# Performance work log

Hardware: AMD Instinct MI355X
Metric: run time of the kernel (lower is better)

The kernel has to match this reference:

```python
import jax, jax.numpy as jnp
import numpy as np

B, S, D, H = 4, 2048, 1024, 16
HD = D // H  # head dim = 64


def setup_inputs() -> dict:
    key = jax.random.key(0)
    ks = jax.random.split(key, 11)
    sc = 1.0 / np.sqrt(D)
    return {
        "q": jax.random.normal(ks[0], (B, S, D), jnp.float32),
        "k": jax.random.normal(ks[1], (B, S, D), jnp.float32),
        "v": jax.random.normal(ks[2], (B, S, D), jnp.float32),
        "w_q": jax.random.normal(ks[3], (D, D), jnp.float32) * sc,
        "b_q": jnp.zeros((D,), jnp.float32),
        "w_k": jax.random.normal(ks[4], (D, D), jnp.float32) * sc,
        "b_k": jnp.zeros((D,), jnp.float32),
        "w_v": jax.random.normal(ks[5], (D, D), jnp.float32) * sc,
        "b_v": jnp.zeros((D,), jnp.float32),
        "w_fc": jax.random.normal(ks[6], (D, D), jnp.float32) * sc,
        "b_fc": jnp.zeros((D,), jnp.float32),
    }


def reference(q, k, v, w_q, b_q, w_k, b_k, w_v, b_v, w_fc, b_fc):
    scale = jnp.asarray(np.sqrt(HD), q.dtype)
    # QKV projections: [B,S,D] @ [D,D]^T (torch Linear: x @ W^T + b)
    Q = (q @ w_q.T + b_q).reshape(B, S, H, HD).transpose(0, 2, 1, 3)  # [B,H,S,HD]
    K = (k @ w_k.T + b_k).reshape(B, S, H, HD).transpose(0, 2, 1, 3)
    V = (v @ w_v.T + b_v).reshape(B, S, H, HD).transpose(0, 2, 1, 3)
    energy = jnp.einsum('bhqd,bhkd->bhqk', Q, K) / scale  # [B,H,S,S]
    attn = jax.nn.softmax(energy, axis=-1)  # dropout is identity in eval / p=0
    x = jnp.einsum('bhqk,bhkd->bhqd', attn, V)  # [B,H,S,HD]
    x = x.transpose(0, 2, 1, 3).reshape(B, S, D)
    return x @ w_fc.T + b_fc
```

## Files before the change

### kernel.cpp

```cpp
#include <hip/hip_runtime.h>
#include <stdint.h>

#define BN 4
#define SEQ 2048
#define DM 1024
#define NH 16
#define HD 64
#define ROWS (BN*SEQ)

typedef float  f32x4  __attribute__((ext_vector_type(4)));
typedef __bf16 bf16x8 __attribute__((ext_vector_type(8)));
typedef __bf16 bf16x4 __attribute__((ext_vector_type(4)));

__device__ inline bf16x8 cvt8(const float* __restrict__ src) {
    float4 x0 = *(const float4*)src;
    float4 x1 = *(const float4*)(src + 4);
    bf16x8 r;
    r[0] = (__bf16)x0.x; r[1] = (__bf16)x0.y; r[2] = (__bf16)x0.z; r[3] = (__bf16)x0.w;
    r[4] = (__bf16)x1.x; r[5] = (__bf16)x1.y; r[6] = (__bf16)x1.z; r[7] = (__bf16)x1.w;
    return r;
}

__device__ inline void gl_lds16(const void* g, void* l) {
    __builtin_amdgcn_global_load_lds((const __attribute__((address_space(1))) uint32_t*)g,
                                     (__attribute__((address_space(3))) uint32_t*)l, 16, 0, 0);
}

__global__ __launch_bounds__(256) void cast3(
    const float* __restrict__ a0, const float* __restrict__ a1, const float* __restrict__ a2,
    __bf16* __restrict__ o0, __bf16* __restrict__ o1, __bf16* __restrict__ o2, int n8) {
    int t = blockIdx.x * 256 + threadIdx.x;
    if (t >= n8) return;
    const float* in = (blockIdx.y == 0) ? a0 : (blockIdx.y == 1) ? a1 : a2;
    __bf16* out     = (blockIdx.y == 0) ? o0 : (blockIdx.y == 1) ? o1 : o2;
    *(bf16x8*)&out[(size_t)t * 8] = cvt8(&in[(size_t)t * 8]);
}

__global__ __launch_bounds__(256) void cast4(
    const float* __restrict__ a0, const float* __restrict__ a1,
    const float* __restrict__ a2, const float* __restrict__ a3,
    __bf16* __restrict__ o0, __bf16* __restrict__ o1,
    __bf16* __restrict__ o2, __bf16* __restrict__ o3, int n8) {
    int t = blockIdx.x * 256 + threadIdx.x;
    if (t >= n8) return;
    const float* in = (blockIdx.y == 0) ? a0 : (blockIdx.y == 1) ? a1 : (blockIdx.y == 2) ? a2 : a3;
    __bf16* out     = (blockIdx.y == 0) ? o0 : (blockIdx.y == 1) ? o1 : (blockIdx.y == 2) ? o2 : o3;
    *(bf16x8*)&out[(size_t)t * 8] = cvt8(&in[(size_t)t * 8]);
}

#define GEMM_CORE_GLDS(Xp, Wp)                                                     \
    __shared__ __align__(16) __bf16 As[128 * 32];                                  \
    __shared__ __align__(16) __bf16 Bs[128 * 32];                                  \
    const int tid  = threadIdx.x;                                                  \
    const int lane = tid & 63;                                                     \
    const int wave = tid >> 6;                                                     \
    const int wm = (wave >> 1) * 64;                                               \
    const int wn = (wave & 1) * 64;                                                \
    const int c16 = lane & 15;                                                     \
    const int g8  = (lane >> 4) * 8;                                               \
    const int row0 = blockIdx.x * 128;                                             \
    const int col0 = blockIdx.y * 128;                                             \
    f32x4 acc[4][4] = {};                                                          \
    for (int k0 = 0; k0 < DM; k0 += 32) {                                          \
        __syncthreads();                                                           \
        _Pragma("unroll")                                                          \
        for (int h = 0; h < 2; h++) {                                              \
            int cidx = h * 256 + tid;                                              \
            gl_lds16(&Xp[(size_t)(row0 + (cidx >> 2)) * DM + k0 + (cidx & 3) * 8], \
                     &As[(size_t)(h * 256 + wave * 64) * 8]);                      \
            gl_lds16(&Wp[(size_t)(col0 + (cidx >> 2)) * DM + k0 + (cidx & 3) * 8], \
                     &Bs[(size_t)(h * 256 + wave * 64) * 8]);                      \
        }                                                                          \
        __syncthreads();                                                           \
        bf16x8 a[4], bfr[4];                                                       \
        _Pragma("unroll")                                                          \
        for (int i = 0; i < 4; i++) a[i]   = *(const bf16x8*)&As[(wm + i * 16 + c16) * 32 + g8]; \
        _Pragma("unroll")                                                          \
        for (int i = 0; i < 4; i++) bfr[i] = *(const bf16x8*)&Bs[(wn + i * 16 + c16) * 32 + g8]; \
        _Pragma("unroll")                                                          \
        for (int mi = 0; mi < 4; mi++)                                             \
            _Pragma("unroll")                                                      \
            for (int ni = 0; ni < 4; ni++)                                         \
                acc[mi][ni] = __builtin_amdgcn_mfma_f32_16x16x32_bf16(a[mi], bfr[ni], acc[mi][ni], 0, 0, 0); \
    }

__global__ __launch_bounds__(256) void gemm_qk_f(
    const __bf16* __restrict__ qb, const __bf16* __restrict__ kb,
    const __bf16* __restrict__ wqb, const __bf16* __restrict__ wkb,
    const float* __restrict__ bq, const float* __restrict__ bk,
    __bf16* __restrict__ Qp, __bf16* __restrict__ Kp)
{
    const int z = blockIdx.z;
    const __bf16* X = z ? kb : qb;
    const __bf16* W = z ? wkb : wqb;
    const float* bias = z ? bk : bq;
    __bf16* O = z ? Kp : Qp;

    GEMM_CORE_GLDS(X, W)

    #pragma unroll
    for (int mi = 0; mi < 4; mi++) {
        int r0 = row0 + wm + mi * 16 + (lane >> 4) * 4;
        #pragma unroll
        for (int ni = 0; ni < 4; ni++) {
            int col = col0 + wn + ni * 16 + c16;
            float bsv = bias[col];
            int h = col >> 6, d = col & 63;
            #pragma unroll
            for (int i = 0; i < 4; i++) {
                int r = r0 + i; int b = r >> 11, s = r & 2047;
                O[((size_t)(b * NH + h) * SEQ + s) * HD + d] = (__bf16)(acc[mi][ni][i] + bsv);
            }
        }
    }
}

__global__ __launch_bounds__(256) void gemm_v_f(
    const __bf16* __restrict__ vb, const __bf16* __restrict__ wvb,
    const float* __restrict__ bv, __bf16* __restrict__ Vt)
{
    GEMM_CORE_GLDS(vb, wvb)

    #pragma unroll
    for (int mi = 0; mi < 4; mi++) {
        int r0 = row0 + wm + mi * 16 + (lane >> 4) * 4;
        #pragma unroll
        for (int ni = 0; ni < 4; ni++) {
            int col = col0 + wn + ni * 16 + c16;
            float bsv = bv[col];
            int h = col >> 6, d = col & 63;
            int b = r0 >> 11, s0 = r0 & 2047;
            size_t base = ((size_t)((b * NH + h) * HD + d)) * SEQ + s0;
            #pragma unroll
            for (int i = 0; i < 4; i++)
                Vt[base + i] = (__bf16)(acc[mi][ni][i] + bsv);
        }
    }
}

__global__ __launch_bounds__(256) void gemm_fc_f(
    const __bf16* __restrict__ Xc, const __bf16* __restrict__ Wfb,
    const float* __restrict__ bias, float* __restrict__ out)
{
    GEMM_CORE_GLDS(Xc, Wfb)

    #pragma unroll
    for (int mi = 0; mi < 4; mi++) {
        int r0 = row0 + wm + mi * 16 + (lane >> 4) * 4;
        #pragma unroll
        for (int ni = 0; ni < 4; ni++) {
            int col = col0 + wn + ni * 16 + c16;
            float bsv = bias[col];
            #pragma unroll
            for (int i = 0; i < 4; i++)
                out[(size_t)(r0 + i) * DM + col] = acc[mi][ni][i] + bsv;
        }
    }
}

__global__ __launch_bounds__(256) void gemm_qk(
    const __bf16* __restrict__ qb, const __bf16* __restrict__ kb,
    const float* __restrict__ wqf, const float* __restrict__ wkf,
    const float* __restrict__ bq, const float* __restrict__ bk,
    __bf16* __restrict__ Qp, __bf16* __restrict__ Kp)
{
    const int z = blockIdx.z;
    const __bf16* X = z ? kb : qb;
    const float* W  = z ? wkf : wqf;
    const float* bias = z ? bk : bq;
    __bf16* O = z ? Kp : Qp;

    __shared__ __align__(16) __bf16 As[128 * 32];
    __shared__ __align__(16) __bf16 Bs[128 * 32];

    const int tid  = threadIdx.x;
    const int lane = tid & 63;
    const int wave = tid >> 6;
    const int wm = (wave >> 1) * 64;
    const int wn = (wave & 1) * 64;
    const int c16 = lane & 15;
    const int g8  = (lane >> 4) * 8;
    const int row0 = blockIdx.x * 128;
    const int col0 = blockIdx.y * 128;
    const int brow = tid >> 1;
    const int bcc  = (tid & 1) * 16;

    f32x4 acc[4][4] = {};
    for (int k0 = 0; k0 < DM; k0 += 32) {
        __syncthreads();
        #pragma unroll
        for (int h = 0; h < 2; h++) {
            int cidx = h * 256 + tid;
            gl_lds16(&X[(size_t)(row0 + (cidx >> 2)) * DM + k0 + (cidx & 3) * 8],
                     &As[(size_t)(h * 256 + wave * 64) * 8]);
        }
        *(bf16x8*)&Bs[brow * 32 + bcc]     = cvt8(&W[(size_t)(col0 + brow) * DM + k0 + bcc]);
        *(bf16x8*)&Bs[brow * 32 + bcc + 8] = cvt8(&W[(size_t)(col0 + brow) * DM + k0 + bcc + 8]);
        __syncthreads();

        bf16x8 a[4], bfr[4];
        #pragma unroll
        for (int i = 0; i < 4; i++) a[i]   = *(const bf16x8*)&As[(wm + i * 16 + c16) * 32 + g8];
        #pragma unroll
        for (int i = 0; i < 4; i++) bfr[i] = *(const bf16x8*)&Bs[(wn + i * 16 + c16) * 32 + g8];
        #pragma unroll
        for (int mi = 0; mi < 4; mi++)
            #pragma unroll
            for (int ni = 0; ni < 4; ni++)
                acc[mi][ni] = __builtin_amdgcn_mfma_f32_16x16x32_bf16(a[mi], bfr[ni], acc[mi][ni], 0, 0, 0);
    }

    #pragma unroll
    for (int mi = 0; mi < 4; mi++) {
        int r0 = row0 + wm + mi * 16 + (lane >> 4) * 4;
        #pragma unroll
        for (int ni = 0; ni < 4; ni++) {
            int col = col0 + wn + ni * 16 + c16;
            float bsv = bias[col];
            int h = col >> 6, d = col & 63;
            #pragma unroll
            for (int i = 0; i < 4; i++) {
                int r = r0 + i; int b = r >> 11, s = r & 2047;
                O[((size_t)(b * NH + h) * SEQ + s) * HD + d] = (__bf16)(acc[mi][ni][i] + bsv);
            }
        }
    }
}

__global__ __launch_bounds__(256) void gemm_v(
    const float* __restrict__ vf, const float* __restrict__ wvf,
    const float* __restrict__ bv, __bf16* __restrict__ Vt)
{
    __shared__ __align__(16) __bf16 As[128 * 32];
    __shared__ __align__(16) __bf16 Bs[128 * 32];

    const int tid  = threadIdx.x;
    const int lane = tid & 63;
    const int wave = tid >> 6;
    const int wm = (wave >> 1) * 64;
    const int wn = (wave & 1) * 64;
    const int c16 = lane & 15;
    const int g8  = (lane >> 4) * 8;
    const int row0 = blockIdx.x * 128;
    const int col0 = blockIdx.y * 128;
    const int brow = tid >> 1;
    const int bcc  = (tid & 1) * 16;

    f32x4 acc[4][4] = {};
    for (int k0 = 0; k0 < DM; k0 += 32) {
        __syncthreads();
        *(bf16x8*)&As[brow * 32 + bcc]     = cvt8(&vf[(size_t)(row0 + brow) * DM + k0 + bcc]);
        *(bf16x8*)&As[brow * 32 + bcc + 8] = cvt8(&vf[(size_t)(row0 + brow) * DM + k0 + bcc + 8]);
        *(bf16x8*)&Bs[brow * 32 + bcc]     = cvt8(&wvf[(size_t)(col0 + brow) * DM + k0 + bcc]);
        *(bf16x8*)&Bs[brow * 32 + bcc + 8] = cvt8(&wvf[(size_t)(col0 + brow) * DM + k0 + bcc + 8]);
        __syncthreads();

        bf16x8 a[4], bfr[4];
        #pragma unroll
        for (int i = 0; i < 4; i++) a[i]   = *(const bf16x8*)&As[(wm + i * 16 + c16) * 32 + g8];
        #pragma unroll
        for (int i = 0; i < 4; i++) bfr[i] = *(const bf16x8*)&Bs[(wn + i * 16 + c16) * 32 + g8];
        #pragma unroll
        for (int mi = 0; mi < 4; mi++)
            #pragma unroll
            for (int ni = 0; ni < 4; ni++)
                acc[mi][ni] = __builtin_amdgcn_mfma_f32_16x16x32_bf16(a[mi], bfr[ni], acc[mi][ni], 0, 0, 0);
    }

    #pragma unroll
    for (int mi = 0; mi < 4; mi++) {
        int r0 = row0 + wm + mi * 16 + (lane >> 4) * 4;
        #pragma unroll
        for (int ni = 0; ni < 4; ni++) {
            int col = col0 + wn + ni * 16 + c16;
            float bsv = bv[col];
            int h = col >> 6, d = col & 63;
            int b = r0 >> 11, s0 = r0 & 2047;
            size_t base = ((size_t)((b * NH + h) * HD + d)) * SEQ + s0;
            #pragma unroll
            for (int i = 0; i < 4; i++)
                Vt[base + i] = (__bf16)(acc[mi][ni][i] + bsv);
        }
    }
}

__global__ __launch_bounds__(256) void gemm_fc(
    const __bf16* __restrict__ Xc, const float* __restrict__ Wf,
    const float* __restrict__ bias, float* __restrict__ out)
{
    __shared__ __align__(16) __bf16 As[128 * 32];
    __shared__ __align__(16) __bf16 Bs[128 * 32];

    const int tid  = threadIdx.x;
    const int lane = tid & 63;
    const int wave = tid >> 6;
    const int wm = (wave >> 1) * 64;
    const int wn = (wave & 1) * 64;
    const int c16 = lane & 15;
    const int g8  = (lane >> 4) * 8;
    const int row0 = blockIdx.x * 128;
    const int col0 = blockIdx.y * 128;
    const int brow = tid >> 1;
    const int bcc  = (tid & 1) * 16;

    f32x4 acc[4][4] = {};
    for (int k0 = 0; k0 < DM; k0 += 32) {
        __syncthreads();
        #pragma unroll
        for (int h = 0; h < 2; h++) {
            int cidx = h * 256 + tid;
            gl_lds16(&Xc[(size_t)(row0 + (cidx >> 2)) * DM + k0 + (cidx & 3) * 8],
                     &As[(size_t)(h * 256 + wave * 64) * 8]);
        }
        *(bf16x8*)&Bs[brow * 32 + bcc]     = cvt8(&Wf[(size_t)(col0 + brow) * DM + k0 + bcc]);
        *(bf16x8*)&Bs[brow * 32 + bcc + 8] = cvt8(&Wf[(size_t)(col0 + brow) * DM + k0 + bcc + 8]);
        __syncthreads();

        bf16x8 a[4], bfr[4];
        #pragma unroll
        for (int i = 0; i < 4; i++) a[i]   = *(const bf16x8*)&As[(wm + i * 16 + c16) * 32 + g8];
        #pragma unroll
        for (int i = 0; i < 4; i++) bfr[i] = *(const bf16x8*)&Bs[(wn + i * 16 + c16) * 32 + g8];
        #pragma unroll
        for (int mi = 0; mi < 4; mi++)
            #pragma unroll
            for (int ni = 0; ni < 4; ni++)
                acc[mi][ni] = __builtin_amdgcn_mfma_f32_16x16x32_bf16(a[mi], bfr[ni], acc[mi][ni], 0, 0, 0);
    }

    #pragma unroll
    for (int mi = 0; mi < 4; mi++) {
        int r0 = row0 + wm + mi * 16 + (lane >> 4) * 4;
        #pragma unroll
        for (int ni = 0; ni < 4; ni++) {
            int col = col0 + wn + ni * 16 + c16;
            float bsv = bias[col];
            #pragma unroll
            for (int i = 0; i < 4; i++)
                out[(size_t)(r0 + i) * DM + col] = acc[mi][ni][i] + bsv;
        }
    }
}

__global__ __launch_bounds__(256, 4) void attn_kernel(
    const __bf16* __restrict__ Qp, const __bf16* __restrict__ Kp,
    const __bf16* __restrict__ Vt, __bf16* __restrict__ ctx)
{
    __shared__ __align__(16) __bf16 Ks[64 * 64];
    __shared__ __align__(16) __bf16 Vs[64 * 64];
    __shared__ __align__(16) __bf16 Ps[4][32 * 64];

    const int tid  = threadIdx.x;
    const int lane = tid & 63;
    const int w    = tid >> 6;
    const int bh   = blockIdx.y;
    const int q0   = blockIdx.x * 128 + w * 32;

    const __bf16* Qb = Qp + (size_t)bh * SEQ * HD;
    const __bf16* Kb = Kp + (size_t)bh * SEQ * HD;
    const __bf16* Vb = Vt + (size_t)bh * HD * SEQ;

    const int c16 = lane & 15;
    const int g   = lane >> 4;
    const int sw  = c16 & 7;

    bf16x8 qf[2][2];
    #pragma unroll
    for (int qs = 0; qs < 2; qs++)
        #pragma unroll
        for (int kc = 0; kc < 2; kc++)
            qf[qs][kc] = *(const bf16x8*)&Qb[(size_t)(q0 + qs * 16 + c16) * HD + kc * 32 + g * 8];

    float lp[2] = {0.f, 0.f};
    f32x4 o[4][2] = {};
    const float SC = 0.18033688f;

    const int srow = (w * 16) + (lane >> 3);
    const int sj   = (lane & 7) ^ (lane >> 3);

    for (int kt = 0; kt < SEQ / 64; kt++) {
        const int k0 = kt * 64;
        __syncthreads();
        #pragma unroll
        for (int h = 0; h < 2; h++) {
            int r = srow + h * 8;
            gl_lds16(&Kb[(size_t)(k0 + r) * HD + sj * 8], &Ks[(size_t)(w * 16 + h * 8) * 64]);
            gl_lds16(&Vb[(size_t)r * SEQ + k0 + sj * 8],  &Vs[(size_t)(w * 16 + h * 8) * 64]);
        }
        __syncthreads();

        f32x4 sc[4][2] = {};
        #pragma unroll
        for (int t = 0; t < 4; t++) {
            #pragma unroll
            for (int kc = 0; kc < 2; kc++) {
                bf16x8 kf = *(const bf16x8*)&Ks[(t * 16 + c16) * 64 + ((kc * 4 + g) ^ sw) * 8];
                sc[t][0] = __builtin_amdgcn_mfma_f32_16x16x32_bf16(kf, qf[0][kc], sc[t][0], 0, 0, 0);
                sc[t][1] = __builtin_amdgcn_mfma_f32_16x16x32_bf16(kf, qf[1][kc], sc[t][1], 0, 0, 0);
            }
        }

        #pragma unroll
        for (int qs = 0; qs < 2; qs++) {
            float ps = 0.f;
            #pragma unroll
            for (int t = 0; t < 4; t++) {
                bf16x4 pk;
                #pragma unroll
                for (int i = 0; i < 4; i++) {
                    float pv = exp2f(sc[t][qs][i] * SC);
                    ps += pv;
                    pk[i] = (__bf16)pv;
                }
                *(bf16x4*)&Ps[w][(qs * 16 + c16) * 64 + ((2 * t + (g >> 1)) ^ sw) * 8 + (g & 1) * 4] = pk;
            }
            lp[qs] += ps;
        }

        bf16x8 pf[2][2];
        #pragma unroll
        for (int qs = 0; qs < 2; qs++)
            #pragma unroll
            for (int kc = 0; kc < 2; kc++)
                pf[qs][kc] = *(const bf16x8*)&Ps[w][(qs * 16 + c16) * 64 + ((kc * 4 + g) ^ sw) * 8];

        #pragma unroll
        for (int t = 0; t < 4; t++) {
            #pragma unroll
            for (int kc = 0; kc < 2; kc++) {
                bf16x8 vfr = *(const bf16x8*)&Vs[(t * 16 + c16) * 64 + ((kc * 4 + g) ^ sw) * 8];
                o[t][0] = __builtin_amdgcn_mfma_f32_16x16x32_bf16(vfr, pf[0][kc], o[t][0], 0, 0, 0);
                o[t][1] = __builtin_amdgcn_mfma_f32_16x16x32_bf16(vfr, pf[1][kc], o[t][1], 0, 0, 0);
            }
        }
    }

    const int hh = bh & (NH - 1);
    const int bb = bh >> 4;
    #pragma unroll
    for (int qs = 0; qs < 2; qs++) {
        float l = lp[qs];
        l += __shfl_xor(l, 16, 64);
        l += __shfl_xor(l, 32, 64);
        float inv = 1.f / l;
        int s = q0 + qs * 16 + c16;
        #pragma unroll
        for (int t = 0; t < 4; t++) {
            bf16x4 ov;
            #pragma unroll
            for (int i = 0; i < 4; i++) ov[i] = (__bf16)(o[t][qs][i] * inv);
            *(bf16x4*)&ctx[((size_t)(bb * SEQ + s)) * DM + hh * HD + t * 16 + g * 4] = ov;
        }
    }
}

extern "C" void kernel_launch(void* const* d_in, const int* in_sizes, int n_in,
                              void* d_out, int out_size, void* d_ws, size_t ws_size,
                              hipStream_t stream) {
    const float* q    = (const float*)d_in[0];
    const float* k    = (const float*)d_in[1];
    const float* v    = (const float*)d_in[2];
    const float* w_q  = (const float*)d_in[3];
    const float* b_q  = (const float*)d_in[4];
    const float* w_k  = (const float*)d_in[5];
    const float* b_k  = (const float*)d_in[6];
    const float* w_v  = (const float*)d_in[7];
    const float* b_v  = (const float*)d_in[8];
    const float* w_fc = (const float*)d_in[9];
    const float* b_fc = (const float*)d_in[10];
    float* out = (float*)d_out;

    __bf16* qb = (__bf16*)d_out;
    __bf16* kb = qb + (size_t)ROWS * DM;

    char* p = (char*)d_ws;
    auto alloc = [&](size_t bytes) { char* r = p; p += (bytes + 255) & ~(size_t)255; return r; };
    const size_t XSZ = (size_t)ROWS * DM * 2;
    const size_t WSZ = (size_t)DM * DM * 2;

    __bf16* Qp  = (__bf16*)alloc(XSZ);
    __bf16* Kp  = (__bf16*)alloc(XSZ);
    __bf16* Vt  = (__bf16*)alloc(XSZ);
    __bf16* ctx = (__bf16*)alloc(XSZ);

    const size_t base_need = (size_t)(p - (char*)d_ws);
    const size_t fast_need = base_need + 4 * (WSZ + 256);

    const int n8x = ROWS * DM / 8;
    const int n8w = DM * DM / 8;

    __bf16* vb = Qp;

    cast3<<<dim3(n8x / 256, 3), 256, 0, stream>>>(q, k, v, qb, kb, vb, n8x);

    if (ws_size >= fast_need) {
        __bf16* wqb  = (__bf16*)alloc(WSZ);
        __bf16* wkb  = (__bf16*)alloc(WSZ);
        __bf16* wvb  = (__bf16*)alloc(WSZ);
        __bf16* wfcb = (__bf16*)alloc(WSZ);

        cast4<<<dim3(n8w / 256, 4), 256, 0, stream>>>(
            w_q, w_k, w_v, w_fc, wqb, wkb, wvb, wfcb, n8w);

        gemm_v_f<<<dim3(ROWS / 128, DM / 128), 256, 0, stream>>>(vb, wvb, b_v, Vt);
        gemm_qk_f<<<dim3(ROWS / 128, DM / 128, 2), 256, 0, stream>>>(
            qb, kb, wqb, wkb, b_q, b_k, Qp, Kp);

        attn_kernel<<<dim3(SEQ / 128, BN * NH), 256, 0, stream>>>(Qp, Kp, Vt, ctx);

        gemm_fc_f<<<dim3(ROWS / 128, DM / 128), 256, 0, stream>>>(ctx, wfcb, b_fc, out);
    } else {
        gemm_v<<<dim3(ROWS / 128, DM / 128), 256, 0, stream>>>(v, w_v, b_v, Vt);
        gemm_qk<<<dim3(ROWS / 128, DM / 128, 2), 256, 0, stream>>>(
            qb, kb, w_q, w_k, b_q, b_k, Qp, Kp);

        attn_kernel<<<dim3(SEQ / 128, BN * NH), 256, 0, stream>>>(Qp, Kp, Vt, ctx);

        gemm_fc<<<dim3(ROWS / 128, DM / 128), 256, 0, stream>>>(ctx, w_fc, b_fc, out);
    }
}
```

Measured before the change: 365.6 us.

## Rewrite attention with 32x32 MFMA, register-resident P, and double-buffered K/V

```diff
diff --git a/kernel.cpp b/kernel.cpp
--- a/kernel.cpp
+++ b/kernel.cpp
@@ -9,8 +9,13 @@
 #define ROWS (BN*SEQ)
 
 typedef float  f32x4  __attribute__((ext_vector_type(4)));
+typedef float  f32x16 __attribute__((ext_vector_type(16)));
 typedef __bf16 bf16x8 __attribute__((ext_vector_type(8)));
 typedef __bf16 bf16x4 __attribute__((ext_vector_type(4)));
+typedef __bf16 bf16x2 __attribute__((ext_vector_type(2)));
+typedef unsigned int u32x4 __attribute__((ext_vector_type(4)));
+
+#define QSCALE 0.18033688f
 
 __device__ inline bf16x8 cvt8(const float* __restrict__ src) {
     float4 x0 = *(const float4*)src;
@@ -95,6 +100,7 @@
     const __bf16* W = z ? wkb : wqb;
     const float* bias = z ? bk : bq;
     __bf16* O = z ? Kp : Qp;
+    const float qsc = z ? 1.0f : QSCALE;
 
     GEMM_CORE_GLDS(X, W)
 
@@ -109,7 +115,7 @@
             #pragma unroll
             for (int i = 0; i < 4; i++) {
                 int r = r0 + i; int b = r >> 11, s = r & 2047;
-                O[((size_t)(b * NH + h) * SEQ + s) * HD + d] = (__bf16)(acc[mi][ni][i] + bsv);
+                O[((size_t)(b * NH + h) * SEQ + s) * HD + d] = (__bf16)((acc[mi][ni][i] + bsv) * qsc);
             }
         }
     }
@@ -169,6 +175,7 @@
     const float* W  = z ? wkf : wqf;
     const float* bias = z ? bk : bq;
     __bf16* O = z ? Kp : Qp;
+    const float qsc = z ? 1.0f : QSCALE;
 
     __shared__ __align__(16) __bf16 As[128 * 32];
     __shared__ __align__(16) __bf16 Bs[128 * 32];
@@ -221,7 +228,7 @@
             #pragma unroll
             for (int i = 0; i < 4; i++) {
                 int r = r0 + i; int b = r >> 11, s = r & 2047;
-                O[((size_t)(b * NH + h) * SEQ + s) * HD + d] = (__bf16)(acc[mi][ni][i] + bsv);
+                O[((size_t)(b * NH + h) * SEQ + s) * HD + d] = (__bf16)((acc[mi][ni][i] + bsv) * qsc);
             }
         }
     }
@@ -342,13 +349,37 @@
     }
 }
 
-__global__ __launch_bounds__(256, 4) void attn_kernel(
+#define SOFTMAX_PACK(SV, PA0, PA1) do {                                            \
+    float p[16]; float ps = 0.f;                                                   \
+    _Pragma("unroll")                                                              \
+    for (int r = 0; r < 16; r++) { float pv = exp2f(SV[r]); p[r] = pv; ps += pv; } \
+    lp += ps;                                                                      \
+    unsigned pw[8];                                                                \
+    _Pragma("unroll")                                                              \
+    for (int i = 0; i < 8; i++) {                                                  \
+        bf16x2 t; t[0] = (__bf16)p[2*i]; t[1] = (__bf16)p[2*i+1];                  \
+        pw[i] = __builtin_bit_cast(unsigned, t);                                   \
+    }                                                                              \
+    unsigned e0 = (unsigned)__shfl_xor((int)pw[0], 32, 64);                        \
+    unsigned e1 = (unsigned)__shfl_xor((int)pw[1], 32, 64);                        \
+    unsigned e2 = (unsigned)__shfl_xor((int)pw[2], 32, 64);                        \
+    unsigned e3 = (unsigned)__shfl_xor((int)pw[3], 32, 64);                        \
+    unsigned e4 = (unsigned)__shfl_xor((int)pw[4], 32, 64);                        \
+    unsigned e5 = (unsigned)__shfl_xor((int)pw[5], 32, 64);                        \
+    unsigned e6 = (unsigned)__shfl_xor((int)pw[6], 32, 64);                        \
+    unsigned e7 = (unsigned)__shfl_xor((int)pw[7], 32, 64);                        \
+    u32x4 wlo = { hi ? e2 : pw[0], hi ? e3 : pw[1], hi ? pw[2] : e0, hi ? pw[3] : e1 }; \
+    u32x4 whi = { hi ? e6 : pw[4], hi ? e7 : pw[5], hi ? pw[6] : e4, hi ? pw[7] : e5 }; \
+    PA0 = __builtin_bit_cast(bf16x8, wlo);                                         \
+    PA1 = __builtin_bit_cast(bf16x8, whi);                                         \
+} while (0)
+
+__global__ __launch_bounds__(256) void attn_kernel(
     const __bf16* __restrict__ Qp, const __bf16* __restrict__ Kp,
     const __bf16* __restrict__ Vt, __bf16* __restrict__ ctx)
 {
-    __shared__ __align__(16) __bf16 Ks[64 * 64];
-    __shared__ __align__(16) __bf16 Vs[64 * 64];
-    __shared__ __align__(16) __bf16 Ps[4][32 * 64];
+    __shared__ __align__(16) __bf16 Ks[2][64 * 64];
+    __shared__ __align__(16) __bf16 Vs[2][64 * 64];
 
     const int tid  = threadIdx.x;
     const int lane = tid & 63;
@@ -360,97 +391,86 @@
     const __bf16* Kb = Kp + (size_t)bh * SEQ * HD;
     const __bf16* Vb = Vt + (size_t)bh * HD * SEQ;
 
-    const int c16 = lane & 15;
-    const int g   = lane >> 4;
-    const int sw  = c16 & 7;
-
-    bf16x8 qf[2][2];
-    #pragma unroll
-    for (int qs = 0; qs < 2; qs++)
-        #pragma unroll
-        for (int kc = 0; kc < 2; kc++)
-            qf[qs][kc] = *(const bf16x8*)&Qb[(size_t)(q0 + qs * 16 + c16) * HD + kc * 32 + g * 8];
-
-    float lp[2] = {0.f, 0.f};
-    f32x4 o[4][2] = {};
-    const float SC = 0.18033688f;
-
-    const int srow = (w * 16) + (lane >> 3);
+    const int c32 = lane & 31;
+    const int hi  = lane >> 5;
+    const int sw  = c32 & 7;
+
+    bf16x8 qf[4];
+    #pragma unroll
+    for (int kc = 0; kc < 4; kc++)
+        qf[kc] = *(const bf16x8*)&Qb[(size_t)(q0 + c32) * HD + kc * 16 + hi * 8];
+
+    f32x16 o0 = {}, o1 = {};
+    float lp = 0.f;
+
+    const int srow = w * 16 + (lane >> 3);
     const int sj   = (lane & 7) ^ (lane >> 3);
 
-    for (int kt = 0; kt < SEQ / 64; kt++) {
+    auto stage = [&](int kt, int buf) {
         const int k0 = kt * 64;
-        __syncthreads();
         #pragma unroll
         for (int h = 0; h < 2; h++) {
             int r = srow + h * 8;
-            gl_lds16(&Kb[(size_t)(k0 + r) * HD + sj * 8], &Ks[(size_t)(w * 16 + h * 8) * 64]);
-            gl_lds16(&Vb[(size_t)r * SEQ + k0 + sj * 8],  &Vs[(size_t)(w * 16 + h * 8) * 64]);
-        }
-        __syncthreads();
-
-        f32x4 sc[4][2] = {};
-        #pragma unroll
-        for (int t = 0; t < 4; t++) {
-            #pragma unroll
-            for (int kc = 0; kc < 2; kc++) {
-                bf16x8 kf = *(const bf16x8*)&Ks[(t * 16 + c16) * 64 + ((kc * 4 + g) ^ sw) * 8];
-                sc[t][0] = __builtin_amdgcn_mfma_f32_16x16x32_bf16(kf, qf[0][kc], sc[t][0], 0, 0, 0);
-                sc[t][1] = __builtin_amdgcn_mfma_f32_16x16x32_bf16(kf, qf[1][kc], sc[t][1], 0, 0, 0);
-            }
-        }
-
-        #pragma unroll
-        for (int qs = 0; qs < 2; qs++) {
-            float ps = 0.f;
-            #pragma unroll
-            for (int t = 0; t < 4; t++) {
-                bf16x4 pk;
-                #pragma unroll
-                for (int i = 0; i < 4; i++) {
-                    float pv = exp2f(sc[t][qs][i] * SC);
-                    ps += pv;
-                    pk[i] = (__bf16)pv;
-                }
-                *(bf16x4*)&Ps[w][(qs * 16 + c16) * 64 + ((2 * t + (g >> 1)) ^ sw) * 8 + (g & 1) * 4] = pk;
-            }
-            lp[qs] += ps;
-        }
-
-        bf16x8 pf[2][2];
-        #pragma unroll
-        for (int qs = 0; qs < 2; qs++)
-            #pragma unroll
-            for (int kc = 0; kc < 2; kc++)
-                pf[qs][kc] = *(const bf16x8*)&Ps[w][(qs * 16 + c16) * 64 + ((kc * 4 + g) ^ sw) * 8];
-
-        #pragma unroll
-        for (int t = 0; t < 4; t++) {
-            #pragma unroll
-            for (int kc = 0; kc < 2; kc++) {
-                bf16x8 vfr = *(const bf16x8*)&Vs[(t * 16 + c16) * 64 + ((kc * 4 + g) ^ sw) * 8];
-                o[t][0] = __builtin_amdgcn_mfma_f32_16x16x32_bf16(vfr, pf[0][kc], o[t][0], 0, 0, 0);
-                o[t][1] = __builtin_amdgcn_mfma_f32_16x16x32_bf16(vfr, pf[1][kc], o[t][1], 0, 0, 0);
-            }
-        }
-    }
-
+            gl_lds16(&Kb[(size_t)(k0 + r) * HD + sj * 8], &Ks[buf][(w * 16 + h * 8) * 64]);
+            gl_lds16(&Vb[(size_t)r * SEQ + k0 + sj * 8],  &Vs[buf][(w * 16 + h * 8) * 64]);
+        }
+    };
+
+    const int NT = SEQ / 64;
+    stage(0, 0);
+    int cur = 0;
+
+    for (int kt = 0; kt < NT; kt++) {
+        __syncthreads();
+        if (kt + 1 < NT) stage(kt + 1, cur ^ 1);
+
+        const __bf16* ksb = &Ks[cur][0];
+        const __bf16* vsb = &Vs[cur][0];
+
+        f32x16 s0v = {}, s1v = {};
+        __builtin_amdgcn_s_setprio(1);
+        #pragma unroll
+        for (int kc = 0; kc < 4; kc++) {
+            bf16x8 kf0 = *(const bf16x8*)&ksb[(c32)      * 64 + (((kc << 1) | hi) ^ sw) * 8];
+            bf16x8 kf1 = *(const bf16x8*)&ksb[(32 + c32) * 64 + (((kc << 1) | hi) ^ sw) * 8];
+            s0v = __builtin_amdgcn_mfma_f32_32x32x16_bf16(kf0, qf[kc], s0v, 0, 0, 0);
+            s1v = __builtin_amdgcn_mfma_f32_32x32x16_bf16(kf1, qf[kc], s1v, 0, 0, 0);
+        }
+        __builtin_amdgcn_s_setprio(0);
+
+        bf16x8 pa[4];
+        SOFTMAX_PACK(s0v, pa[0], pa[1]);
+        SOFTMAX_PACK(s1v, pa[2], pa[3]);
+
+        __builtin_amdgcn_s_setprio(1);
+        #pragma unroll
+        for (int ks = 0; ks < 4; ks++) {
+            bf16x8 vf0 = *(const bf16x8*)&vsb[(c32)      * 64 + (((ks << 1) | hi) ^ sw) * 8];
+            bf16x8 vf1 = *(const bf16x8*)&vsb[(32 + c32) * 64 + (((ks << 1) | hi) ^ sw) * 8];
+            o0 = __builtin_amdgcn_mfma_f32_32x32x16_bf16(vf0, pa[ks], o0, 0, 0, 0);
+            o1 = __builtin_amdgcn_mfma_f32_32x32x16_bf16(vf1, pa[ks], o1, 0, 0, 0);
+        }
+        __builtin_amdgcn_s_setprio(0);
+
+        cur ^= 1;
+    }
+
+    float l = lp + __shfl_xor(lp, 32, 64);
+    float inv = 1.f / l;
     const int hh = bh & (NH - 1);
     const int bb = bh >> 4;
-    #pragma unroll
-    for (int qs = 0; qs < 2; qs++) {
-        float l = lp[qs];
-        l += __shfl_xor(l, 16, 64);
-        l += __shfl_xor(l, 32, 64);
-        float inv = 1.f / l;
-        int s = q0 + qs * 16 + c16;
-        #pragma unroll
-        for (int t = 0; t < 4; t++) {
-            bf16x4 ov;
-            #pragma unroll
-            for (int i = 0; i < 4; i++) ov[i] = (__bf16)(o[t][qs][i] * inv);
-            *(bf16x4*)&ctx[((size_t)(bb * SEQ + s)) * DM + hh * HD + t * 16 + g * 4] = ov;
-        }
+    const int s  = q0 + c32;
+    __bf16* cb = &ctx[((size_t)(bb * SEQ + s)) * DM + hh * HD];
+    #pragma unroll
+    for (int u = 0; u < 4; u++) {
+        bf16x4 ov0, ov1;
+        #pragma unroll
+        for (int i = 0; i < 4; i++) {
+            ov0[i] = (__bf16)(o0[4 * u + i] * inv);
+            ov1[i] = (__bf16)(o1[4 * u + i] * inv);
+        }
+        *(bf16x4*)&cb[u * 8 + hi * 4]      = ov0;
+        *(bf16x4*)&cb[32 + u * 8 + hi * 4] = ov1;
     }
 }
 
```

Result: slower. 393.8 us (+7.7%).
